# Kernel tuning notes

Measured on AMD Instinct MI355X. Metric: run time of the kernel, lower is better.

Reference implementation:

```python
import jax, jax.numpy as jnp
import numpy as np

C = 4        # num_case (3) + coreference (1)
H = 128      # self.hidden_size
D = 768      # bert hidden size
B, S = 2, 384


def setup_inputs() -> dict:
    key = jax.random.key(0)
    ks = jax.random.split(key, 9)
    sc = 0.02
    return {
        "sequence_output": jax.random.normal(ks[0], (B, S, D), jnp.float32),
        "base_score": jax.random.uniform(ks[1], (B, S, C, S), jnp.float32),
        "W_prd_w": jax.random.normal(ks[2], (D, C * H), jnp.float32) * sc,
        "W_prd_b": jnp.zeros((C * H,), jnp.float32),
        "U_arg_w": jax.random.normal(ks[3], (D, C * H), jnp.float32) * sc,
        "U_arg_b": jnp.zeros((C * H,), jnp.float32),
        "W_mid": jax.random.normal(ks[4], (H * (C + 2), H), jnp.float32) * sc,
        "b_mid": jnp.zeros((H,), jnp.float32),
        "w_out": jax.random.normal(ks[5], (H,), jnp.float32) * sc,
    }


def reference(sequence_output, base_score, W_prd_w, W_prd_b, U_arg_w, U_arg_b, W_mid, b_mid, w_out):
    b, s, _ = sequence_output.shape
    # projections (dropout = identity in eval)
    h_p = (sequence_output @ W_prd_w + W_prd_b).reshape(b, s, C, H)   # [B,S,C,H]
    h_a = (sequence_output @ U_arg_w + U_arg_b).reshape(b, s, C, H)   # [B,S,C,H]
    # weighted_sum over argument positions: base_score[b,prd,case,arg]
    ref = jnp.einsum("bach,bpca->bpch", h_a, base_score).reshape(b, s, C * H)  # [B,S,C*H]
    # mid_layer(tanh(cat[prd_rep, h_a, ref])) == sum of three block matmuls,
    # since tanh is elementwise on each concatenated block.
    W1, W2, W3 = W_mid[:H], W_mid[H:2 * H], W_mid[2 * H:]
    t_prd = jnp.einsum("bpch,hk->bpck", jnp.tanh(h_p), W1)   # [B,Sp,C,H]
    t_arg = jnp.einsum("bach,hk->back", jnp.tanh(h_a), W2)   # [B,Sa,C,H]
    t_ref = jnp.tanh(ref) @ W3                                # [B,Sp,H]
    h_mid = (t_prd[:, :, None, :, :] + t_arg[:, None, :, :, :]
             + t_ref[:, :, None, None, :] + b_mid)            # [B,Sp,Sa,C,H]
    out = jnp.tanh(h_mid) @ w_out                             # [B,Sp,Sa,C]
    return out.transpose(0, 1, 3, 2)                          # [B,Sp,C,Sa]
```

## Files before the change

### kernel.cpp

```cpp
#include <hip/hip_runtime.h>
#include <hip/hip_bf16.h>


#define C2 2.885390081777927f

typedef __attribute__((ext_vector_type(8))) __bf16 bf16x8;
typedef __attribute__((ext_vector_type(8))) unsigned short ushort8;
typedef __attribute__((ext_vector_type(4))) float float4v;
typedef __attribute__((ext_vector_type(2))) float float2v;

__device__ __forceinline__ unsigned short f2bf(float f) {
  unsigned int u = __float_as_uint(f);
  u += 0x7fffu + ((u >> 16) & 1u);
  return (unsigned short)(u >> 16);
}

__device__ __forceinline__ float fast_tanh(float x) {
  float e = __builtin_amdgcn_exp2f(C2 * x);
  return 1.0f - 2.0f * __builtin_amdgcn_rcpf(1.0f + e);
}

__global__ __launch_bounds__(256) void gemm_bf16(
    const float* __restrict__ A, int lda, long aSb, long aSc,
    const float* __restrict__ B0, int ldb, long bSb, long bSc,
    const float* __restrict__ B1,
    const float* __restrict__ bias0, const float* __restrict__ bias1,
    int M, int N, int K,
    float* __restrict__ outF, unsigned short* __restrict__ outB,
    float* __restrict__ outT, int ldc, long cSb, long cSc, float scale,
    int fmask, int bmask, int tmask)
{
  __shared__ unsigned short Alds[64 * 40];
  __shared__ unsigned short Blds[64 * 40];

  const int tid = threadIdx.x;
  const int z = blockIdx.z;
  const float* B = (z == 1 && B1) ? B1 : B0;
  const float* bias = (z == 1 && B1) ? bias1 : bias0;
  const long aoff = (long)(z >> 2) * aSb + (long)(z & 3) * aSc;
  const long boff = (long)(z >> 2) * bSb + (long)(z & 3) * bSc;
  const long coff = (long)(z >> 2) * cSb + (long)(z & 3) * cSc;
  const int bn0 = blockIdx.x * 64;
  const int bm0 = blockIdx.y * 64;
  const int wid = tid >> 6, lane = tid & 63;
  const int wm0 = (wid >> 1) * 32, wn0 = (wid & 1) * 32;
  const int col16 = lane & 15, quad = lane >> 4;

  float4v acc[2][2];
#pragma unroll
  for (int i = 0; i < 2; ++i)
#pragma unroll
    for (int j = 0; j < 2; ++j) acc[i][j] = (float4v)(0.f);

  const int ar = tid >> 2, ac = (tid & 3) * 8;
  const int bk = tid >> 3, bn = (tid & 7) * 8;

  const float* Abase = A + aoff + (size_t)(bm0 + ar) * lda + ac;
  const float* Bbase = B + boff + (size_t)bk * ldb + bn0 + bn;

  float4 a0 = ((const float4*)Abase)[0], a1 = ((const float4*)Abase)[1];
  float4 b0 = ((const float4*)Bbase)[0], b1 = ((const float4*)Bbase)[1];

  for (int k0 = 0; k0 < K; k0 += 32) {
    __syncthreads();
    {
      ushort8 o;
      o[0] = f2bf(a0.x); o[1] = f2bf(a0.y); o[2] = f2bf(a0.z); o[3] = f2bf(a0.w);
      o[4] = f2bf(a1.x); o[5] = f2bf(a1.y); o[6] = f2bf(a1.z); o[7] = f2bf(a1.w);
      *(ushort8*)&Alds[ar * 40 + ac] = o;
      float vv[8] = {b0.x, b0.y, b0.z, b0.w, b1.x, b1.y, b1.z, b1.w};
#pragma unroll
      for (int j = 0; j < 8; ++j) Blds[(bn + j) * 40 + bk] = f2bf(vv[j]);
    }
    __syncthreads();

    if (k0 + 32 < K) {
      const float4* An = (const float4*)(Abase + k0 + 32);
      const float4* Bn = (const float4*)(Bbase + (size_t)(k0 + 32) * ldb);
      a0 = An[0]; a1 = An[1];
      b0 = Bn[0]; b1 = Bn[1];
    }

    bf16x8 afrag[2], bfrag[2];
#pragma unroll
    for (int i = 0; i < 2; ++i)
      afrag[i] = __builtin_bit_cast(bf16x8,
          *(const ushort8*)&Alds[(wm0 + i * 16 + col16) * 40 + quad * 8]);
#pragma unroll
    for (int j = 0; j < 2; ++j)
      bfrag[j] = __builtin_bit_cast(bf16x8,
          *(const ushort8*)&Blds[(wn0 + j * 16 + col16) * 40 + quad * 8]);
#pragma unroll
    for (int i = 0; i < 2; ++i)
#pragma unroll
      for (int j = 0; j < 2; ++j)
        acc[i][j] = __builtin_amdgcn_mfma_f32_16x16x32_bf16(
            afrag[i], bfrag[j], acc[i][j], 0, 0, 0);
  }

  const bool wF = outF && ((fmask >> z) & 1);
  const bool wB = outB && ((bmask >> z) & 1);
  const bool wT = outT && ((tmask >> z) & 1);

#pragma unroll
  for (int j = 0; j < 2; ++j) {
    const int gcol = bn0 + wn0 + j * 16 + col16;
    const float bv = bias ? bias[gcol] : 0.f;
#pragma unroll
    for (int i = 0; i < 2; ++i) {
#pragma unroll
      for (int r = 0; r < 4; ++r) {
        const int grow = bm0 + wm0 + i * 16 + quad * 4 + r;
        const float x = acc[i][j][r] + bv;
        const size_t cidx = (size_t)grow * ldc + gcol + coff;
        if (wF) outF[cidx] = scale * x;
        if (wB) outB[cidx] = f2bf(scale * x);
        if (wT) outT[cidx] = fast_tanh(x);
      }
    }
  }
}

__global__ __launch_bounds__(128) void phase2(
    const float* __restrict__ tprd, const unsigned short* __restrict__ targ,
    const float* __restrict__ tref, const float* __restrict__ bmid,
    const float* __restrict__ wout, float* __restrict__ out)
{
  __shared__ unsigned int Gs[128 * 34];
  __shared__ float Es[8 * 128];
  __shared__ float Ws[128];

  const int tid = threadIdx.x;
  const int p0 = blockIdx.x * 8, a0 = blockIdx.y * 128;
  const int b = blockIdx.z >> 2, c = blockIdx.z & 3;

  if (tid < 32) {
    float4 w = ((const float4*)wout)[tid];
    Ws[tid * 4 + 0] = -2.f * w.x; Ws[tid * 4 + 1] = -2.f * w.y;
    Ws[tid * 4 + 2] = -2.f * w.z; Ws[tid * 4 + 3] = -2.f * w.w;
  }
#pragma unroll
  for (int it = 0; it < 8; ++it) {
    int idx = it * 128 + tid;
    int p = idx >> 7, k = idx & 127;
    int row = b * 384 + p0 + p;
    float f = tprd[(size_t)(row * 4 + c) * 128 + k] +
              tref[(size_t)row * 128 + k] + C2 * bmid[k];
    Es[idx] = __builtin_amdgcn_exp2f(f);
  }
  float sw = 0.f;
  for (int k4 = 0; k4 < 32; ++k4) {
    float4 w = ((const float4*)wout)[k4];
    sw += w.x + w.y + w.z + w.w;
  }

  float2v accA[8], accB[8];
#pragma unroll
  for (int p = 0; p < 8; ++p) { accA[p] = (float2v)(0.f); accB[p] = (float2v)(0.f); }

  const unsigned int* gsrc = (const unsigned int*)targ;
  const size_t grow_base = (size_t)((b * 384 + a0) * 4 + c) * 64;

  for (int h = 0; h < 2; ++h) {
    __syncthreads();
#pragma unroll 8
    for (int it = 0; it < 32; ++it) {
      int idx = it * 128 + tid;
      int r = idx >> 5, col = idx & 31;
      Gs[r * 34 + col] = gsrc[grow_base + (size_t)r * 256 + h * 32 + col];
    }
    __syncthreads();

    const unsigned int* g = &Gs[tid * 34];
    const int kb = h * 64;
    for (int j = 0; j < 16; ++j) {
      uint2 gp = *(const uint2*)(g + j * 2);
      float eg0 = __builtin_amdgcn_exp2f(__uint_as_float(gp.x << 16));
      float eg1 = __builtin_amdgcn_exp2f(__uint_as_float(gp.x & 0xffff0000u));
      float eg2 = __builtin_amdgcn_exp2f(__uint_as_float(gp.y << 16));
      float eg3 = __builtin_amdgcn_exp2f(__uint_as_float(gp.y & 0xffff0000u));
      float2v w01 = *(const float2v*)&Ws[kb + j * 4];
      float2v w23 = *(const float2v*)&Ws[kb + j * 4 + 2];
#pragma unroll
      for (int p = 0; p < 8; ++p) {
        float4 ef = *(const float4*)&Es[p * 128 + kb + j * 4];
        float2v e01 = {ef.x * eg0, ef.y * eg1};
        float2v e23 = {ef.z * eg2, ef.w * eg3};
        float2v d01 = e01 + 1.f;
        float2v d23 = e23 + 1.f;
        float2v r01 = {__builtin_amdgcn_rcpf(d01.x), __builtin_amdgcn_rcpf(d01.y)};
        float2v r23 = {__builtin_amdgcn_rcpf(d23.x), __builtin_amdgcn_rcpf(d23.y)};
        accA[p] += w01 * r01;
        accB[p] += w23 * r23;
      }
    }
  }

  const size_t ob = (size_t)((b * 384 + p0) * 4 + c) * 384 + a0 + tid;
#pragma unroll
  for (int p = 0; p < 8; ++p)
    out[ob + (size_t)p * 1536] = sw + accA[p].x + accA[p].y + accB[p].x + accB[p].y;
}

extern "C" void kernel_launch(void* const* d_in, const int* in_sizes, int n_in,
                              void* d_out, int out_size, void* d_ws, size_t ws_size,
                              hipStream_t stream) {
  (void)in_sizes; (void)n_in; (void)out_size; (void)ws_size;
  const float* seq  = (const float*)d_in[0];
  const float* base = (const float*)d_in[1];
  const float* Wp   = (const float*)d_in[2];
  const float* Wpb  = (const float*)d_in[3];
  const float* Ua   = (const float*)d_in[4];
  const float* Uab  = (const float*)d_in[5];
  const float* Wmid = (const float*)d_in[6];
  const float* bmid = (const float*)d_in[7];
  const float* wout = (const float*)d_in[8];
  float* out = (float*)d_out;

  float* ws = (float*)d_ws;
  float* tanh_hp  = ws;
  float* tanh_ref = ws + 786432;
  float* h_a      = ws + 1179648;
  float* tprd_s   = ws + 1572864;
  float* tref_s   = ws + 1966080;
  unsigned short* targ_s = (unsigned short*)(ws + 2064384);

  dim3 blk(256);
  gemm_bf16<<<dim3(8, 12, 2), blk, 0, stream>>>(
      seq, 768, 0, 0, Wp, 512, 0, 0, Ua, Wpb, Uab, 768, 512, 768,
       h_a - 393216, nullptr,
       tanh_hp, 512, 0, 393216, 1.f, 0b10, 0, 0b11);
  gemm_bf16<<<dim3(2, 6, 8), blk, 0, stream>>>(
      base, 1536, 589824, 384, h_a, 512, 196608, 128, nullptr, nullptr, nullptr,
      384, 128, 384, nullptr, nullptr, tanh_ref, 512, 196608, 128, 1.f,
      0, 0, 0xFF);
  gemm_bf16<<<dim3(2, 48, 2), blk, 0, stream>>>(
      tanh_hp, 128, 0, 393216, Wmid, 128, 0, 16384, nullptr, nullptr, nullptr,
      3072, 128, 128, tprd_s, targ_s, nullptr, 128, 0, 0, C2,
      0b01, 0b10, 0);
  gemm_bf16<<<dim3(2, 12, 1), blk, 0, stream>>>(
      tanh_ref, 512, 0, 0, Wmid + 32768, 128, 0, 0, nullptr, nullptr, nullptr,
      768, 128, 512, tref_s, nullptr, nullptr, 128, 0, 0, C2, 1, 0, 0);
  phase2<<<dim3(48, 3, 8), dim3(128), 0, stream>>>(
      tprd_s, targ_s, tref_s, bmid, wout, out);
}
```

Before: 156.5 us.

## Fuse projection and mid GEMMs into fewer launches, merge tanh reciprocals

Replaces the generic four-launch GEMM pipeline with two specialised kernels. The first runs both projections and zeroes the tref buffer. The second fuses the ref weighted sum, its tanh and the W3 projection, accumulating into tref with atomics, and runs the W1/W2 projections in the same launch. In phase2 the inner loop pairs two tanh terms over a common denominator, halving the reciprocal count and using fmas. This cuts launch count and intermediate global traffic. The cost is float atomics, which make summation order non-deterministic, and a possible overflow risk from multiplying two exponentials.

Result: faster. 140.5 us (-10.2%).

```diff
diff --git a/kernel.cpp b/kernel.cpp
--- a/kernel.cpp
+++ b/kernel.cpp
@@ -7,7 +7,6 @@
 typedef __attribute__((ext_vector_type(8))) __bf16 bf16x8;
 typedef __attribute__((ext_vector_type(8))) unsigned short ushort8;
 typedef __attribute__((ext_vector_type(4))) float float4v;
-typedef __attribute__((ext_vector_type(2))) float float2v;
 
 __device__ __forceinline__ unsigned short f2bf(float f) {
   unsigned int u = __float_as_uint(f);
@@ -20,46 +19,17 @@
   return 1.0f - 2.0f * __builtin_amdgcn_rcpf(1.0f + e);
 }
 
-__global__ __launch_bounds__(256) void gemm_bf16(
-    const float* __restrict__ A, int lda, long aSb, long aSc,
-    const float* __restrict__ B0, int ldb, long bSb, long bSc,
-    const float* __restrict__ B1,
-    const float* __restrict__ bias0, const float* __restrict__ bias1,
-    int M, int N, int K,
-    float* __restrict__ outF, unsigned short* __restrict__ outB,
-    float* __restrict__ outT, int ldc, long cSb, long cSc, float scale,
-    int fmask, int bmask, int tmask)
+__device__ __forceinline__ void gemm_core(
+    const float* __restrict__ Abase, int lda,
+    const float* __restrict__ Bbase, int ldb, int K,
+    unsigned short* Alds, unsigned short* Blds,
+    int ar, int ac, int bk, int bn,
+    int wm0, int wn0, int col16, int quad, float4v acc[2][2])
 {
-  __shared__ unsigned short Alds[64 * 40];
-  __shared__ unsigned short Blds[64 * 40];
-
-  const int tid = threadIdx.x;
-  const int z = blockIdx.z;
-  const float* B = (z == 1 && B1) ? B1 : B0;
-  const float* bias = (z == 1 && B1) ? bias1 : bias0;
-  const long aoff = (long)(z >> 2) * aSb + (long)(z & 3) * aSc;
-  const long boff = (long)(z >> 2) * bSb + (long)(z & 3) * bSc;
-  const long coff = (long)(z >> 2) * cSb + (long)(z & 3) * cSc;
-  const int bn0 = blockIdx.x * 64;
-  const int bm0 = blockIdx.y * 64;
-  const int wid = tid >> 6, lane = tid & 63;
-  const int wm0 = (wid >> 1) * 32, wn0 = (wid & 1) * 32;
-  const int col16 = lane & 15, quad = lane >> 4;
-
-  float4v acc[2][2];
-#pragma unroll
-  for (int i = 0; i < 2; ++i)
-#pragma unroll
-    for (int j = 0; j < 2; ++j) acc[i][j] = (float4v)(0.f);
-
-  const int ar = tid >> 2, ac = (tid & 3) * 8;
-  const int bk = tid >> 3, bn = (tid & 7) * 8;
-
-  const float* Abase = A + aoff + (size_t)(bm0 + ar) * lda + ac;
-  const float* Bbase = B + boff + (size_t)bk * ldb + bn0 + bn;
-
-  float4 a0 = ((const float4*)Abase)[0], a1 = ((const float4*)Abase)[1];
-  float4 b0 = ((const float4*)Bbase)[0], b1 = ((const float4*)Bbase)[1];
+  const float* Ap = Abase + (size_t)ar * lda + ac;
+  const float* Bp = Bbase + (size_t)bk * ldb + bn;
+  float4 a0 = ((const float4*)Ap)[0], a1 = ((const float4*)Ap)[1];
+  float4 b0 = ((const float4*)Bp)[0], b1 = ((const float4*)Bp)[1];
 
   for (int k0 = 0; k0 < K; k0 += 32) {
     __syncthreads();
@@ -73,14 +43,11 @@
       for (int j = 0; j < 8; ++j) Blds[(bn + j) * 40 + bk] = f2bf(vv[j]);
     }
     __syncthreads();
-
     if (k0 + 32 < K) {
-      const float4* An = (const float4*)(Abase + k0 + 32);
-      const float4* Bn = (const float4*)(Bbase + (size_t)(k0 + 32) * ldb);
-      a0 = An[0]; a1 = An[1];
-      b0 = Bn[0]; b1 = Bn[1];
-    }
-
+      const float4* An = (const float4*)(Ap + k0 + 32);
+      const float4* Bn = (const float4*)(Bp + (size_t)(k0 + 32) * ldb);
+      a0 = An[0]; a1 = An[1]; b0 = Bn[0]; b1 = Bn[1];
+    }
     bf16x8 afrag[2], bfrag[2];
 #pragma unroll
     for (int i = 0; i < 2; ++i)
@@ -97,26 +64,169 @@
         acc[i][j] = __builtin_amdgcn_mfma_f32_16x16x32_bf16(
             afrag[i], bfrag[j], acc[i][j], 0, 0, 0);
   }
-
-  const bool wF = outF && ((fmask >> z) & 1);
-  const bool wB = outB && ((bmask >> z) & 1);
-  const bool wT = outT && ((tmask >> z) & 1);
-
+}
+
+__global__ __launch_bounds__(256) void g1_dual(
+    const float* __restrict__ seq, const float* __restrict__ Wp,
+    const float* __restrict__ Ua, const float* __restrict__ Wpb,
+    const float* __restrict__ Uab, float* __restrict__ tanh_out,
+    float* __restrict__ h_a, float* __restrict__ tref_clear)
+{
+  const int z = blockIdx.z;
+  if (z == 2) {
+    int idx = ((blockIdx.y * 8 + blockIdx.x) * 256 + threadIdx.x) * 4;
+    *(float4*)&tref_clear[idx] = float4{0.f, 0.f, 0.f, 0.f};
+    return;
+  }
+  __shared__ unsigned short Alds[64 * 40];
+  __shared__ unsigned short Blds[64 * 40];
+  const int tid = threadIdx.x;
+  const int bn0 = blockIdx.x * 64, bm0 = blockIdx.y * 64;
+  const int wid = tid >> 6, lane = tid & 63;
+  const int wm0 = (wid >> 1) * 32, wn0 = (wid & 1) * 32;
+  const int col16 = lane & 15, quad = lane >> 4;
+  const float* B = z ? Ua : Wp;
+  const float* bias = z ? Uab : Wpb;
+
+  float4v acc[2][2];
+#pragma unroll
+  for (int i = 0; i < 2; ++i)
+#pragma unroll
+    for (int j = 0; j < 2; ++j) acc[i][j] = (float4v)(0.f);
+
+  gemm_core(seq + (size_t)bm0 * 768, 768, B + bn0, 512, 768,
+            Alds, Blds, tid >> 2, (tid & 3) * 8, tid >> 3, (tid & 7) * 8,
+            wm0, wn0, col16, quad, acc);
+
+  float* tout = tanh_out + (size_t)z * 393216;
 #pragma unroll
   for (int j = 0; j < 2; ++j) {
     const int gcol = bn0 + wn0 + j * 16 + col16;
-    const float bv = bias ? bias[gcol] : 0.f;
-#pragma unroll
-    for (int i = 0; i < 2; ++i) {
+    const float bv = bias[gcol];
+#pragma unroll
+    for (int i = 0; i < 2; ++i)
 #pragma unroll
       for (int r = 0; r < 4; ++r) {
         const int grow = bm0 + wm0 + i * 16 + quad * 4 + r;
         const float x = acc[i][j][r] + bv;
-        const size_t cidx = (size_t)grow * ldc + gcol + coff;
-        if (wF) outF[cidx] = scale * x;
-        if (wB) outB[cidx] = f2bf(scale * x);
-        if (wT) outT[cidx] = fast_tanh(x);
+        const size_t cidx = (size_t)grow * 512 + gcol;
+        tout[cidx] = fast_tanh(x);
+        if (z == 1) h_a[cidx] = x;
       }
+  }
+}
+
+__global__ __launch_bounds__(256) void fused_mid(
+    const float* __restrict__ base, const float* __restrict__ h_a,
+    const float* __restrict__ tanh_h, const float* __restrict__ Wmid,
+    float* __restrict__ tprd_s, unsigned short* __restrict__ targ_s,
+    float* __restrict__ tref_s)
+{
+  __shared__ unsigned short Alds[64 * 40];
+  __shared__ unsigned short Blds[64 * 40];
+  __shared__ unsigned short TA[64 * 72];
+  __shared__ unsigned short TB[128 * 72];
+
+  const int tid = threadIdx.x;
+  const int bid = blockIdx.x;
+  const int wid = tid >> 6, lane = tid & 63;
+  const int wm0 = (wid >> 1) * 32, wn0 = (wid & 1) * 32;
+  const int col16 = lane & 15, quad = lane >> 4;
+  const int ar = tid >> 2, ac = (tid & 3) * 8;
+  const int bk = tid >> 3, bn = (tid & 7) * 8;
+
+  float4v acc[2][2];
+#pragma unroll
+  for (int i = 0; i < 2; ++i)
+#pragma unroll
+    for (int j = 0; j < 2; ++j) acc[i][j] = (float4v)(0.f);
+
+  if (bid < 96) {
+    const int z = bid / 12, rem = bid % 12;
+    const int b = z >> 2, c = z & 3;
+    const int y = rem >> 1, x = rem & 1;
+    const float* A = base + (size_t)b * 589824 + c * 384 + (size_t)(y * 64) * 1536;
+    const float* Bm = h_a + (size_t)b * 196608 + c * 128 + x * 64;
+    gemm_core(A, 1536, Bm, 512, 384, Alds, Blds, ar, ac, bk, bn,
+              wm0, wn0, col16, quad, acc);
+
+#pragma unroll
+    for (int j = 0; j < 2; ++j)
+#pragma unroll
+      for (int i = 0; i < 2; ++i)
+#pragma unroll
+        for (int r = 0; r < 4; ++r)
+          TA[(wm0 + i * 16 + quad * 4 + r) * 72 + wn0 + j * 16 + col16] =
+              f2bf(fast_tanh(acc[i][j][r]));
+    {
+      const float* W3p = Wmid + 32768 + (size_t)(c * 128 + x * 64) * 128;
+      const int kr = tid >> 2, nb = (tid & 3) * 32;
+#pragma unroll
+      for (int q = 0; q < 8; ++q) {
+        float4 v = *(const float4*)(W3p + (size_t)kr * 128 + nb + q * 4);
+        TB[(nb + q * 4 + 0) * 72 + kr] = f2bf(v.x);
+        TB[(nb + q * 4 + 1) * 72 + kr] = f2bf(v.y);
+        TB[(nb + q * 4 + 2) * 72 + kr] = f2bf(v.z);
+        TB[(nb + q * 4 + 3) * 72 + kr] = f2bf(v.w);
+      }
+    }
+    __syncthreads();
+
+    const int mh = wid & 1, nh = wid >> 1;
+    float4v acc2[2][4];
+#pragma unroll
+    for (int i = 0; i < 2; ++i)
+#pragma unroll
+      for (int j = 0; j < 4; ++j) acc2[i][j] = (float4v)(0.f);
+#pragma unroll
+    for (int ks = 0; ks < 2; ++ks) {
+      bf16x8 af[2], bf[4];
+#pragma unroll
+      for (int i = 0; i < 2; ++i)
+        af[i] = __builtin_bit_cast(bf16x8,
+            *(const ushort8*)&TA[(mh * 32 + i * 16 + col16) * 72 + ks * 32 + quad * 8]);
+#pragma unroll
+      for (int j = 0; j < 4; ++j)
+        bf[j] = __builtin_bit_cast(bf16x8,
+            *(const ushort8*)&TB[(nh * 64 + j * 16 + col16) * 72 + ks * 32 + quad * 8]);
+#pragma unroll
+      for (int i = 0; i < 2; ++i)
+#pragma unroll
+        for (int j = 0; j < 4; ++j)
+          acc2[i][j] = __builtin_amdgcn_mfma_f32_16x16x32_bf16(
+              af[i], bf[j], acc2[i][j], 0, 0, 0);
+    }
+#pragma unroll
+    for (int j = 0; j < 4; ++j) {
+      const int gcol = nh * 64 + j * 16 + col16;
+#pragma unroll
+      for (int i = 0; i < 2; ++i)
+#pragma unroll
+        for (int r = 0; r < 4; ++r) {
+          const int grow = b * 384 + y * 64 + mh * 32 + i * 16 + quad * 4 + r;
+          atomicAdd(&tref_s[(size_t)grow * 128 + gcol], C2 * acc2[i][j][r]);
+        }
+    }
+  } else {
+    const int idx = bid - 96;
+    const int x = idx & 1, y = (idx >> 1) % 48, z = idx / 96;
+    const float* A = tanh_h + (size_t)z * 393216 + (size_t)(y * 64) * 128;
+    const float* Bm = Wmid + z * 16384 + x * 64;
+    gemm_core(A, 128, Bm, 128, 128, Alds, Blds, ar, ac, bk, bn,
+              wm0, wn0, col16, quad, acc);
+#pragma unroll
+    for (int j = 0; j < 2; ++j) {
+      const int gcol = x * 64 + wn0 + j * 16 + col16;
+#pragma unroll
+      for (int i = 0; i < 2; ++i)
+#pragma unroll
+        for (int r = 0; r < 4; ++r) {
+          const int grow = y * 64 + wm0 + i * 16 + quad * 4 + r;
+          const float v = C2 * acc[i][j][r];
+          const size_t cidx = (size_t)grow * 128 + gcol;
+          if (z == 0) tprd_s[cidx] = v;
+          else        targ_s[cidx] = f2bf(v);
+        }
     }
   }
 }
@@ -154,9 +264,9 @@
     sw += w.x + w.y + w.z + w.w;
   }
 
-  float2v accA[8], accB[8];
-#pragma unroll
-  for (int p = 0; p < 8; ++p) { accA[p] = (float2v)(0.f); accB[p] = (float2v)(0.f); }
+  float acc01[8], acc23[8];
+#pragma unroll
+  for (int p = 0; p < 8; ++p) { acc01[p] = 0.f; acc23[p] = 0.f; }
 
   const unsigned int* gsrc = (const unsigned int*)targ;
   const size_t grow_base = (size_t)((b * 384 + a0) * 4 + c) * 64;
@@ -173,25 +283,27 @@
 
     const unsigned int* g = &Gs[tid * 34];
     const int kb = h * 64;
+#pragma unroll 2
     for (int j = 0; j < 16; ++j) {
       uint2 gp = *(const uint2*)(g + j * 2);
       float eg0 = __builtin_amdgcn_exp2f(__uint_as_float(gp.x << 16));
       float eg1 = __builtin_amdgcn_exp2f(__uint_as_float(gp.x & 0xffff0000u));
       float eg2 = __builtin_amdgcn_exp2f(__uint_as_float(gp.y << 16));
       float eg3 = __builtin_amdgcn_exp2f(__uint_as_float(gp.y & 0xffff0000u));
-      float2v w01 = *(const float2v*)&Ws[kb + j * 4];
-      float2v w23 = *(const float2v*)&Ws[kb + j * 4 + 2];
+      float4 wq = *(const float4*)&Ws[kb + j * 4];
 #pragma unroll
       for (int p = 0; p < 8; ++p) {
         float4 ef = *(const float4*)&Es[p * 128 + kb + j * 4];
-        float2v e01 = {ef.x * eg0, ef.y * eg1};
-        float2v e23 = {ef.z * eg2, ef.w * eg3};
-        float2v d01 = e01 + 1.f;
-        float2v d23 = e23 + 1.f;
-        float2v r01 = {__builtin_amdgcn_rcpf(d01.x), __builtin_amdgcn_rcpf(d01.y)};
-        float2v r23 = {__builtin_amdgcn_rcpf(d23.x), __builtin_amdgcn_rcpf(d23.y)};
-        accA[p] += w01 * r01;
-        accB[p] += w23 * r23;
+        float d0 = fmaf(ef.x, eg0, 1.f);
+        float d1 = fmaf(ef.y, eg1, 1.f);
+        float d2 = fmaf(ef.z, eg2, 1.f);
+        float d3 = fmaf(ef.w, eg3, 1.f);
+        float r01 = __builtin_amdgcn_rcpf(d0 * d1);
+        float r23 = __builtin_amdgcn_rcpf(d2 * d3);
+        float n01 = fmaf(wq.y, d0, wq.x * d1);
+        float n23 = fmaf(wq.w, d2, wq.z * d3);
+        acc01[p] = fmaf(n01, r01, acc01[p]);
+        acc23[p] = fmaf(n23, r23, acc23[p]);
       }
     }
   }
@@ -199,7 +311,7 @@
   const size_t ob = (size_t)((b * 384 + p0) * 4 + c) * 384 + a0 + tid;
 #pragma unroll
   for (int p = 0; p < 8; ++p)
-    out[ob + (size_t)p * 1536] = sw + accA[p].x + accA[p].y + accB[p].x + accB[p].y;
+    out[ob + (size_t)p * 1536] = sw + acc01[p] + acc23[p];
 }
 
 extern "C" void kernel_launch(void* const* d_in, const int* in_sizes, int n_in,
@@ -218,29 +330,16 @@
   float* out = (float*)d_out;
 
   float* ws = (float*)d_ws;
-  float* tanh_hp  = ws;
-  float* tanh_ref = ws + 786432;
-  float* h_a      = ws + 1179648;
-  float* tprd_s   = ws + 1572864;
-  float* tref_s   = ws + 1966080;
-  unsigned short* targ_s = (unsigned short*)(ws + 2064384);
-
-  dim3 blk(256);
-  gemm_bf16<<<dim3(8, 12, 2), blk, 0, stream>>>(
-      seq, 768, 0, 0, Wp, 512, 0, 0, Ua, Wpb, Uab, 768, 512, 768,
-       h_a - 393216, nullptr,
-       tanh_hp, 512, 0, 393216, 1.f, 0b10, 0, 0b11);
-  gemm_bf16<<<dim3(2, 6, 8), blk, 0, stream>>>(
-      base, 1536, 589824, 384, h_a, 512, 196608, 128, nullptr, nullptr, nullptr,
-      384, 128, 384, nullptr, nullptr, tanh_ref, 512, 196608, 128, 1.f,
-      0, 0, 0xFF);
-  gemm_bf16<<<dim3(2, 48, 2), blk, 0, stream>>>(
-      tanh_hp, 128, 0, 393216, Wmid, 128, 0, 16384, nullptr, nullptr, nullptr,
-      3072, 128, 128, tprd_s, targ_s, nullptr, 128, 0, 0, C2,
-      0b01, 0b10, 0);
-  gemm_bf16<<<dim3(2, 12, 1), blk, 0, stream>>>(
-      tanh_ref, 512, 0, 0, Wmid + 32768, 128, 0, 0, nullptr, nullptr, nullptr,
-      768, 128, 512, tref_s, nullptr, nullptr, 128, 0, 0, C2, 1, 0, 0);
+  float* tanh_hp = ws;
+  float* h_a     = ws + 786432;
+  float* tprd_s  = ws + 1179648;
+  float* tref_s  = ws + 1572864;
+  unsigned short* targ_s = (unsigned short*)(ws + 1671168);
+
+  g1_dual<<<dim3(8, 12, 3), dim3(256), 0, stream>>>(
+      seq, Wp, Ua, Wpb, Uab, tanh_hp, h_a, tref_s);
+  fused_mid<<<dim3(288), dim3(256), 0, stream>>>(
+      base, h_a, tanh_hp, Wmid, tprd_s, targ_s, tref_s);
   phase2<<<dim3(48, 3, 8), dim3(128), 0, stream>>>(
       tprd_s, targ_s, tref_s, bmid, wout, out);
 }
```
